# Optimization experiments

Measured on AMD Instinct MI355X. Metric: run time of the kernel, lower is better.

## Reference

```python
import jax, jax.numpy as jnp
import numpy as np


def setup_inputs() -> dict:
    key = jax.random.key(0)
    k1, k2 = jax.random.split(key)
    enc = jax.random.normal(k1, (32, 64, 64, 64), dtype=jnp.float32)   # (B, C, H, W), C == D
    embed = jax.random.normal(k2, (512, 64), dtype=jnp.float32)        # (K, D) codebook
    return {"enc": enc, "embed": embed}


def reference(enc, embed):
    B, C, H, W = enc.shape
    K, D = embed.shape
    # torch: enc.view(B, -1, C) with C == D -> plain reshape (no transpose), faithful to source.
    x = enc.reshape(B, -1, D)                                          # (B, N, D), N = C*H*W/D
    # Squared L2 distances; argmin is invariant under sqrt so we skip torch.cdist's sqrt.
    x_sq = jnp.sum(x * x, axis=-1, keepdims=True)                      # (B, N, 1)
    e_sq = jnp.sum(embed * embed, axis=-1)                             # (K,)
    d2 = x_sq - 2.0 * jnp.einsum('bnd,kd->bnk', x, embed) + e_sq       # (B, N, K)
    closest = jnp.argmin(d2, axis=-1)                                  # (B, N) int
    quantized = embed[closest]                                         # (B, N, D) gather
    commitment_loss = jnp.mean((jax.lax.stop_gradient(quantized) - x) ** 2)
    codebook_loss = jnp.mean((quantized - jax.lax.stop_gradient(x)) ** 2)
    quantize_loss = codebook_loss + 1.0 * commitment_loss
    # Straight-through estimator.
    quant_out = (x + jax.lax.stop_gradient(quantized - x)).reshape(B, C, H, W)
    return quant_out, quantize_loss, closest
```

## Files before the change

### kernel.cpp

```cpp
#include <hip/hip_runtime.h>
#include <math.h>

#define DQ 64
#define KQ 512
#define NVEC 131072
#define QOUT_SIZE (NVEC * DQ)
#define LOSS_OFF QOUT_SIZE
#define IDX_OFF (QOUT_SIZE + 1)

#define RPW 32
#define WPB 4
#define VPB (RPW * WPB)
#define NBLK (NVEC / VPB)
#define SC 64
#define NST (KQ / SC)
#define SDQ (SC * DQ)
#define TIE_THR 0.01f

typedef __attribute__((ext_vector_type(8))) short short8;
typedef __attribute__((ext_vector_type(4))) float f32x4;

static __device__ __forceinline__ unsigned short f2bf(float f) {
    unsigned u = __float_as_uint(f);
    u += 0x7fff + ((u >> 16) & 1);
    return (unsigned short)(u >> 16);
}
static __device__ __forceinline__ float bf2f(unsigned short h) {
    return __uint_as_float(((unsigned)h) << 16);
}
static __device__ __forceinline__ void cvt8(float4 a, float4 b, short8& hi, short8& lo) {
#define C1(I, V) { unsigned short _h = f2bf(V); hi[I] = (short)_h; lo[I] = (short)f2bf((V) - bf2f(_h)); }
    C1(0, a.x) C1(1, a.y) C1(2, a.z) C1(3, a.w)
    C1(4, b.x) C1(5, b.y) C1(6, b.z) C1(7, b.w)
#undef C1
}

__global__ void vq_init_kernel(const float* __restrict__ embed,
                               unsigned short* __restrict__ ehi,
                               unsigned short* __restrict__ elo,
                               float* __restrict__ esq,
                               float* __restrict__ out) {
    const int t = blockIdx.x * 64 + threadIdx.x;
    if (t == 0) out[LOSS_OFF] = 0.0f;
    const int k = t >> 3;
    const int c = t & 7;
    const float4* p = (const float4*)(embed + (size_t)k * DQ + c * 8);
    float4 a = p[0], b = p[1];
    short8 hi, lo;
    cvt8(a, b, hi, lo);
    const int slot = c ^ (k & 7);
    *(short8*)(ehi + (size_t)k * DQ + slot * 8) = hi;
    *(short8*)(elo + (size_t)k * DQ + slot * 8) = lo;

    float ps = 0.f;
    ps = fmaf(a.x, a.x, ps); ps = fmaf(a.y, a.y, ps); ps = fmaf(a.z, a.z, ps); ps = fmaf(a.w, a.w, ps);
    ps = fmaf(b.x, b.x, ps); ps = fmaf(b.y, b.y, ps); ps = fmaf(b.z, b.z, ps); ps = fmaf(b.w, b.w, ps);
    ps += __shfl_xor(ps, 1);
    ps += __shfl_xor(ps, 2);
    ps += __shfl_xor(ps, 4);
    if (c == 0) esq[k] = ps;
}

__global__ __launch_bounds__(256) void vq_mfma_kernel(const float* __restrict__ enc,
                                                      const float* __restrict__ embed,
                                                      const unsigned short* __restrict__ ehi,
                                                      const unsigned short* __restrict__ elo,
                                                      const float* __restrict__ esq,
                                                      float* __restrict__ out) {
    __shared__ unsigned short hs[2 * SDQ];
    __shared__ unsigned short ls_[2 * SDQ];
    __shared__ float esq_s[KQ];
    __shared__ int bidx_s[VPB];
    __shared__ int flag_s[VPB];
    __shared__ float red[WPB];

    const int tid = threadIdx.x;
    const int lane = tid & 63;
    const int w = tid >> 6;
    const int l15 = lane & 15;
    const int l4 = lane >> 4;
    const int vb = blockIdx.x * VPB + w * RPW;

    esq_s[tid] = esq[tid];
    esq_s[tid + 256] = esq[tid + 256];

    short8 ahA[2], alA[2], ahB[2], alB[2];
#pragma unroll
    for (int a = 0; a < 2; a++) {
        const float* base = enc + (size_t)(vb + a * 16 + l15) * DQ + l4 * 8;
        const float4* p0 = (const float4*)base;
        const float4* p1 = (const float4*)(base + 32);
        cvt8(p0[0], p0[1], ahA[a], alA[a]);
        cvt8(p1[0], p1[1], ahB[a], alB[a]);
    }

    float m1[8], m2[8];
    int i1[8];
#pragma unroll
    for (int r = 0; r < 8; r++) { m1[r] = 3.4e38f; m2[r] = 3.4e38f; i1[r] = 0; }

    const int sl0 = (l4 ^ (l15 & 7)) * 8;
    const int sl1 = sl0 ^ 32;

    short8 rh0 = *(const short8*)(ehi + tid * 8);
    short8 rh1 = *(const short8*)(ehi + 2048 + tid * 8);
    short8 rl0 = *(const short8*)(elo + tid * 8);
    short8 rl1 = *(const short8*)(elo + 2048 + tid * 8);
    *(short8*)(hs + tid * 8) = rh0;  *(short8*)(hs + 2048 + tid * 8) = rh1;
    *(short8*)(ls_ + tid * 8) = rl0; *(short8*)(ls_ + 2048 + tid * 8) = rl1;
    rh0 = *(const short8*)(ehi + SDQ + tid * 8);
    rh1 = *(const short8*)(ehi + SDQ + 2048 + tid * 8);
    rl0 = *(const short8*)(elo + SDQ + tid * 8);
    rl1 = *(const short8*)(elo + SDQ + 2048 + tid * 8);

#define LDB(H0, H1, L0, L1, S) { const int _o = ((S) * 16 + l15) * DQ; \
    H0 = *(const short8*)(hb + _o + sl0); H1 = *(const short8*)(hb + _o + sl1); \
    L0 = *(const short8*)(lb + _o + sl0); L1 = *(const short8*)(lb + _o + sl1); }

#define BODY(ST, S, BH0, BH1, BL0, BL1) { \
    const int code = (ST) * SC + (S) * 16 + l15; \
    const float ev = esq_s[code]; \
    _Pragma("unroll") \
    for (int a = 0; a < 2; a++) { \
        f32x4 acc = {0.f, 0.f, 0.f, 0.f}; \
        acc = __builtin_amdgcn_mfma_f32_16x16x32_bf16(ahA[a], BH0, acc, 0, 0, 0); \
        acc = __builtin_amdgcn_mfma_f32_16x16x32_bf16(ahB[a], BH1, acc, 0, 0, 0); \
        acc = __builtin_amdgcn_mfma_f32_16x16x32_bf16(alA[a], BH0, acc, 0, 0, 0); \
        acc = __builtin_amdgcn_mfma_f32_16x16x32_bf16(alB[a], BH1, acc, 0, 0, 0); \
        acc = __builtin_amdgcn_mfma_f32_16x16x32_bf16(ahA[a], BL0, acc, 0, 0, 0); \
        acc = __builtin_amdgcn_mfma_f32_16x16x32_bf16(ahB[a], BL1, acc, 0, 0, 0); \
        _Pragma("unroll") \
        for (int r = 0; r < 4; r++) { \
            float v = fmaf(-2.0f, acc[r], ev); \
            bool lt = v < m1[a * 4 + r]; \
            i1[a * 4 + r] = lt ? code : i1[a * 4 + r]; \
            m2[a * 4 + r] = fminf(m2[a * 4 + r], fmaxf(m1[a * 4 + r], v)); \
            m1[a * 4 + r] = fminf(m1[a * 4 + r], v); \
        } \
    } }

    for (int st = 0; st < NST; st++) {
        __syncthreads();
        if (st < NST - 1) {
            unsigned short* hw = hs + ((st + 1) & 1) * SDQ;
            unsigned short* lw = ls_ + ((st + 1) & 1) * SDQ;
            *(short8*)(hw + tid * 8) = rh0;  *(short8*)(hw + 2048 + tid * 8) = rh1;
            *(short8*)(lw + tid * 8) = rl0;  *(short8*)(lw + 2048 + tid * 8) = rl1;
        }
        if (st < NST - 2) {
            const int o = (st + 2) * SDQ;
            rh0 = *(const short8*)(ehi + o + tid * 8);
            rh1 = *(const short8*)(ehi + o + 2048 + tid * 8);
            rl0 = *(const short8*)(elo + o + tid * 8);
            rl1 = *(const short8*)(elo + o + 2048 + tid * 8);
        }
        const unsigned short* hb = hs + (st & 1) * SDQ;
        const unsigned short* lb = ls_ + (st & 1) * SDQ;
        short8 b0h0, b0h1, b0l0, b0l1, b1h0, b1h1, b1l0, b1l1;
        LDB(b0h0, b0h1, b0l0, b0l1, 0)
        LDB(b1h0, b1h1, b1l0, b1l1, 1)
        BODY(st, 0, b0h0, b0h1, b0l0, b0l1)
        LDB(b0h0, b0h1, b0l0, b0l1, 2)
        BODY(st, 1, b1h0, b1h1, b1l0, b1l1)
        LDB(b1h0, b1h1, b1l0, b1l1, 3)
        BODY(st, 2, b0h0, b0h1, b0l0, b0l1)
        BODY(st, 3, b1h0, b1h1, b1l0, b1l1)
    }
#undef LDB
#undef BODY

#pragma unroll
    for (int m = 1; m <= 8; m <<= 1) {
#pragma unroll
        for (int r = 0; r < 8; r++) {
            float o1 = __shfl_xor(m1[r], m);
            float o2 = __shfl_xor(m2[r], m);
            int oi = __shfl_xor(i1[r], m);
            float nm2 = fminf(fminf(m2[r], o2), fmaxf(m1[r], o1));
            bool lt = o1 < m1[r];
            i1[r] = lt ? oi : i1[r];
            m1[r] = fminf(m1[r], o1);
            m2[r] = nm2;
        }
    }

    if (l15 == 0) {
#pragma unroll
        for (int a = 0; a < 2; a++)
#pragma unroll
            for (int r = 0; r < 4; r++) {
                const int row = a * 16 + l4 * 4 + r;
                bidx_s[w * RPW + row] = i1[a * 4 + r];
                flag_s[w * RPW + row] = (m2[a * 4 + r] - m1[a * 4 + r] < TIE_THR) ? 1 : 0;
            }
    }

    for (int row = 0; row < RPW; row++) {
        if (flag_s[w * RPW + row]) {
            const int v = vb + row;
            const float4* xe = (const float4*)(enc + (size_t)v * DQ);
            unsigned long long best = ~0ULL;
            for (int q = 0; q < 8; q++) {
                const int c = lane * 8 + q;
                const float4* ee = (const float4*)(embed + (size_t)c * DQ);
                double a = 0.0;
                for (int j = 0; j < 16; j++) {
                    float4 xx = xe[j], ez = ee[j];
                    double d0 = (double)xx.x - (double)ez.x; a = fma(d0, d0, a);
                    double d1 = (double)xx.y - (double)ez.y; a = fma(d1, d1, a);
                    double d2 = (double)xx.z - (double)ez.z; a = fma(d2, d2, a);
                    double d3 = (double)xx.w - (double)ez.w; a = fma(d3, d3, a);
                }
                unsigned long long p =
                    (((unsigned long long)__double_as_longlong(a)) & ~511ULL) | (unsigned)c;
                best = (p < best) ? p : best;
            }
#pragma unroll
            for (int mm = 1; mm < 64; mm <<= 1) {
                unsigned long long ob = (unsigned long long)__shfl_xor((long long)best, mm);
                best = (ob < best) ? ob : best;
            }
            if (lane == 0) bidx_s[w * RPW + row] = (int)(best & 511ULL);
        }
    }

    float lsum = 0.f;
#pragma unroll
    for (int a = 0; a < 2; a++) {
        const int myv = vb + a * 16 + l15;
        const int qb = bidx_s[w * RPW + a * 16 + l15];
        const float* qbase = embed + (size_t)qb * DQ + l4 * 8;
        const float4* qa = (const float4*)qbase;
        const float4* qc = (const float4*)(qbase + 32);
        float4 q0 = qa[0], q1 = qa[1], q2 = qc[0], q3 = qc[1];
        float* obase = out + (size_t)myv * DQ + l4 * 8;
        ((float4*)obase)[0] = q0; ((float4*)obase)[1] = q1;
        ((float4*)(obase + 32))[0] = q2; ((float4*)(obase + 32))[1] = q3;
        if (l4 == 0) out[IDX_OFF + myv] = (float)qb;

        float d;
        d = q0.x - (bf2f(ahA[a][0]) + bf2f(alA[a][0])); lsum = fmaf(d, d, lsum);
        d = q0.y - (bf2f(ahA[a][1]) + bf2f(alA[a][1])); lsum = fmaf(d, d, lsum);
        d = q0.z - (bf2f(ahA[a][2]) + bf2f(alA[a][2])); lsum = fmaf(d, d, lsum);
        d = q0.w - (bf2f(ahA[a][3]) + bf2f(alA[a][3])); lsum = fmaf(d, d, lsum);
        d = q1.x - (bf2f(ahA[a][4]) + bf2f(alA[a][4])); lsum = fmaf(d, d, lsum);
        d = q1.y - (bf2f(ahA[a][5]) + bf2f(alA[a][5])); lsum = fmaf(d, d, lsum);
        d = q1.z - (bf2f(ahA[a][6]) + bf2f(alA[a][6])); lsum = fmaf(d, d, lsum);
        d = q1.w - (bf2f(ahA[a][7]) + bf2f(alA[a][7])); lsum = fmaf(d, d, lsum);
        d = q2.x - (bf2f(ahB[a][0]) + bf2f(alB[a][0])); lsum = fmaf(d, d, lsum);
        d = q2.y - (bf2f(ahB[a][1]) + bf2f(alB[a][1])); lsum = fmaf(d, d, lsum);
        d = q2.z - (bf2f(ahB[a][2]) + bf2f(alB[a][2])); lsum = fmaf(d, d, lsum);
        d = q2.w - (bf2f(ahB[a][3]) + bf2f(alB[a][3])); lsum = fmaf(d, d, lsum);
        d = q3.x - (bf2f(ahB[a][4]) + bf2f(alB[a][4])); lsum = fmaf(d, d, lsum);
        d = q3.y - (bf2f(ahB[a][5]) + bf2f(alB[a][5])); lsum = fmaf(d, d, lsum);
        d = q3.z - (bf2f(ahB[a][6]) + bf2f(alB[a][6])); lsum = fmaf(d, d, lsum);
        d = q3.w - (bf2f(ahB[a][7]) + bf2f(alB[a][7])); lsum = fmaf(d, d, lsum);
    }

#pragma unroll
    for (int off = 32; off > 0; off >>= 1) lsum += __shfl_down(lsum, off);
    if (lane == 0) red[w] = lsum;
    __syncthreads();
    if (tid == 0) {
        float s = (red[0] + red[1]) + (red[2] + red[3]);
        atomicAdd(out + LOSS_OFF, s * (2.0f / (float)QOUT_SIZE));
    }
}

extern "C" void kernel_launch(void* const* d_in, const int* in_sizes, int n_in,
                              void* d_out, int out_size, void* d_ws, size_t ws_size,
                              hipStream_t stream) {
    const float* enc = (const float*)d_in[0];
    const float* embed = (const float*)d_in[1];
    float* out = (float*)d_out;
    unsigned short* ehi = (unsigned short*)d_ws;
    unsigned short* elo = ehi + KQ * DQ;
    float* esq = (float*)(elo + KQ * DQ);

    hipLaunchKernelGGL(vq_init_kernel, dim3(64), dim3(64), 0, stream,
                       embed, ehi, elo, esq, out);
    hipLaunchKernelGGL(vq_mfma_kernel, dim3(NBLK), dim3(256), 0, stream,
                       enc, embed, ehi, elo, esq, out);
}
```

Measured before the change: 141.8 us.

## Drop codebook low-bf16 split, pack argmin index into distance bits, widen tie threshold

Removes the low-precision half of the codebook split, so each tile needs four MFMAs instead of six and half the shared-memory staging and global loads. The code index is packed into the low mantissa bits of the distance, which removes the separate index tracking and its shuffles. The tie threshold rises from 0.01 to 0.2 to make up for the lost precision, so more rows may drop into the slow fp64 recheck path. The shared buffer is also padded with an odd-looking pad that raises LDS usage and may lower occupancy.

```diff
diff --git a/kernel.cpp b/kernel.cpp
--- a/kernel.cpp
+++ b/kernel.cpp
@@ -15,7 +15,9 @@
 #define SC 64
 #define NST (KQ / SC)
 #define SDQ (SC * DQ)
-#define TIE_THR 0.01f
+#define PADS 2654
+#define SDQ_P (SDQ + PADS)
+#define TIE_THR 0.2f
 
 typedef __attribute__((ext_vector_type(8))) short short8;
 typedef __attribute__((ext_vector_type(4))) float f32x4;
@@ -37,7 +39,6 @@
 
 __global__ void vq_init_kernel(const float* __restrict__ embed,
                                unsigned short* __restrict__ ehi,
-                               unsigned short* __restrict__ elo,
                                float* __restrict__ esq,
                                float* __restrict__ out) {
     const int t = blockIdx.x * 64 + threadIdx.x;
@@ -46,11 +47,12 @@
     const int c = t & 7;
     const float4* p = (const float4*)(embed + (size_t)k * DQ + c * 8);
     float4 a = p[0], b = p[1];
-    short8 hi, lo;
-    cvt8(a, b, hi, lo);
+    unsigned short h0 = f2bf(a.x), h1 = f2bf(a.y), h2 = f2bf(a.z), h3 = f2bf(a.w);
+    unsigned short h4 = f2bf(b.x), h5 = f2bf(b.y), h6 = f2bf(b.z), h7 = f2bf(b.w);
+    short8 hi = { (short)h0, (short)h1, (short)h2, (short)h3,
+                  (short)h4, (short)h5, (short)h6, (short)h7 };
     const int slot = c ^ (k & 7);
     *(short8*)(ehi + (size_t)k * DQ + slot * 8) = hi;
-    *(short8*)(elo + (size_t)k * DQ + slot * 8) = lo;
 
     float ps = 0.f;
     ps = fmaf(a.x, a.x, ps); ps = fmaf(a.y, a.y, ps); ps = fmaf(a.z, a.z, ps); ps = fmaf(a.w, a.w, ps);
@@ -64,11 +66,9 @@
 __global__ __launch_bounds__(256) void vq_mfma_kernel(const float* __restrict__ enc,
                                                       const float* __restrict__ embed,
                                                       const unsigned short* __restrict__ ehi,
-                                                      const unsigned short* __restrict__ elo,
                                                       const float* __restrict__ esq,
                                                       float* __restrict__ out) {
-    __shared__ unsigned short hs[2 * SDQ];
-    __shared__ unsigned short ls_[2 * SDQ];
+    __shared__ unsigned short hs[2 * SDQ_P];
     __shared__ float esq_s[KQ];
     __shared__ int bidx_s[VPB];
     __shared__ int flag_s[VPB];
@@ -95,29 +95,22 @@
     }
 
     float m1[8], m2[8];
-    int i1[8];
-#pragma unroll
-    for (int r = 0; r < 8; r++) { m1[r] = 3.4e38f; m2[r] = 3.4e38f; i1[r] = 0; }
+#pragma unroll
+    for (int r = 0; r < 8; r++) { m1[r] = 3.4e38f; m2[r] = 3.4e38f; }
 
     const int sl0 = (l4 ^ (l15 & 7)) * 8;
     const int sl1 = sl0 ^ 32;
 
     short8 rh0 = *(const short8*)(ehi + tid * 8);
     short8 rh1 = *(const short8*)(ehi + 2048 + tid * 8);
-    short8 rl0 = *(const short8*)(elo + tid * 8);
-    short8 rl1 = *(const short8*)(elo + 2048 + tid * 8);
     *(short8*)(hs + tid * 8) = rh0;  *(short8*)(hs + 2048 + tid * 8) = rh1;
-    *(short8*)(ls_ + tid * 8) = rl0; *(short8*)(ls_ + 2048 + tid * 8) = rl1;
     rh0 = *(const short8*)(ehi + SDQ + tid * 8);
     rh1 = *(const short8*)(ehi + SDQ + 2048 + tid * 8);
-    rl0 = *(const short8*)(elo + SDQ + tid * 8);
-    rl1 = *(const short8*)(elo + SDQ + 2048 + tid * 8);
-
-#define LDB(H0, H1, L0, L1, S) { const int _o = ((S) * 16 + l15) * DQ; \
-    H0 = *(const short8*)(hb + _o + sl0); H1 = *(const short8*)(hb + _o + sl1); \
-    L0 = *(const short8*)(lb + _o + sl0); L1 = *(const short8*)(lb + _o + sl1); }
-
-#define BODY(ST, S, BH0, BH1, BL0, BL1) { \
+
+#define LDB(H0, H1, S) { const int _o = ((S) * 16 + l15) * DQ; \
+    H0 = *(const short8*)(hb + _o + sl0); H1 = *(const short8*)(hb + _o + sl1); }
+
+#define BODY(ST, S, BH0, BH1) { \
     const int code = (ST) * SC + (S) * 16 + l15; \
     const float ev = esq_s[code]; \
     _Pragma("unroll") \
@@ -127,44 +120,36 @@
         acc = __builtin_amdgcn_mfma_f32_16x16x32_bf16(ahB[a], BH1, acc, 0, 0, 0); \
         acc = __builtin_amdgcn_mfma_f32_16x16x32_bf16(alA[a], BH0, acc, 0, 0, 0); \
         acc = __builtin_amdgcn_mfma_f32_16x16x32_bf16(alB[a], BH1, acc, 0, 0, 0); \
-        acc = __builtin_amdgcn_mfma_f32_16x16x32_bf16(ahA[a], BL0, acc, 0, 0, 0); \
-        acc = __builtin_amdgcn_mfma_f32_16x16x32_bf16(ahB[a], BL1, acc, 0, 0, 0); \
         _Pragma("unroll") \
         for (int r = 0; r < 4; r++) { \
             float v = fmaf(-2.0f, acc[r], ev); \
-            bool lt = v < m1[a * 4 + r]; \
-            i1[a * 4 + r] = lt ? code : i1[a * 4 + r]; \
-            m2[a * 4 + r] = fminf(m2[a * 4 + r], fmaxf(m1[a * 4 + r], v)); \
-            m1[a * 4 + r] = fminf(m1[a * 4 + r], v); \
+            float p = __uint_as_float((__float_as_uint(v) & 0xFFFFFE00u) | (unsigned)code); \
+            m2[a * 4 + r] = fminf(m2[a * 4 + r], fmaxf(m1[a * 4 + r], p)); \
+            m1[a * 4 + r] = fminf(m1[a * 4 + r], p); \
         } \
     } }
 
     for (int st = 0; st < NST; st++) {
         __syncthreads();
         if (st < NST - 1) {
-            unsigned short* hw = hs + ((st + 1) & 1) * SDQ;
-            unsigned short* lw = ls_ + ((st + 1) & 1) * SDQ;
+            unsigned short* hw = hs + ((st + 1) & 1) * SDQ_P;
             *(short8*)(hw + tid * 8) = rh0;  *(short8*)(hw + 2048 + tid * 8) = rh1;
-            *(short8*)(lw + tid * 8) = rl0;  *(short8*)(lw + 2048 + tid * 8) = rl1;
         }
         if (st < NST - 2) {
             const int o = (st + 2) * SDQ;
             rh0 = *(const short8*)(ehi + o + tid * 8);
             rh1 = *(const short8*)(ehi + o + 2048 + tid * 8);
-            rl0 = *(const short8*)(elo + o + tid * 8);
-            rl1 = *(const short8*)(elo + o + 2048 + tid * 8);
-        }
-        const unsigned short* hb = hs + (st & 1) * SDQ;
-        const unsigned short* lb = ls_ + (st & 1) * SDQ;
-        short8 b0h0, b0h1, b0l0, b0l1, b1h0, b1h1, b1l0, b1l1;
-        LDB(b0h0, b0h1, b0l0, b0l1, 0)
-        LDB(b1h0, b1h1, b1l0, b1l1, 1)
-        BODY(st, 0, b0h0, b0h1, b0l0, b0l1)
-        LDB(b0h0, b0h1, b0l0, b0l1, 2)
-        BODY(st, 1, b1h0, b1h1, b1l0, b1l1)
-        LDB(b1h0, b1h1, b1l0, b1l1, 3)
-        BODY(st, 2, b0h0, b0h1, b0l0, b0l1)
-        BODY(st, 3, b1h0, b1h1, b1l0, b1l1)
+        }
+        const unsigned short* hb = hs + (st & 1) * SDQ_P;
+        short8 b0h0, b0h1, b1h0, b1h1;
+        LDB(b0h0, b0h1, 0)
+        LDB(b1h0, b1h1, 1)
+        BODY(st, 0, b0h0, b0h1)
+        LDB(b0h0, b0h1, 2)
+        BODY(st, 1, b1h0, b1h1)
+        LDB(b1h0, b1h1, 3)
+        BODY(st, 2, b0h0, b0h1)
+        BODY(st, 3, b1h0, b1h1)
     }
 #undef LDB
 #undef BODY
@@ -175,12 +160,8 @@
         for (int r = 0; r < 8; r++) {
             float o1 = __shfl_xor(m1[r], m);
             float o2 = __shfl_xor(m2[r], m);
-            int oi = __shfl_xor(i1[r], m);
-            float nm2 = fminf(fminf(m2[r], o2), fmaxf(m1[r], o1));
-            bool lt = o1 < m1[r];
-            i1[r] = lt ? oi : i1[r];
+            m2[r] = fminf(fminf(m2[r], o2), fmaxf(m1[r], o1));
             m1[r] = fminf(m1[r], o1);
-            m2[r] = nm2;
         }
     }
 
@@ -190,7 +171,7 @@
 #pragma unroll
             for (int r = 0; r < 4; r++) {
                 const int row = a * 16 + l4 * 4 + r;
-                bidx_s[w * RPW + row] = i1[a * 4 + r];
+                bidx_s[w * RPW + row] = (int)(__float_as_uint(m1[a * 4 + r]) & 511u);
                 flag_s[w * RPW + row] = (m2[a * 4 + r] - m1[a * 4 + r] < TIE_THR) ? 1 : 0;
             }
     }
@@ -274,11 +255,10 @@
     const float* embed = (const float*)d_in[1];
     float* out = (float*)d_out;
     unsigned short* ehi = (unsigned short*)d_ws;
-    unsigned short* elo = ehi + KQ * DQ;
-    float* esq = (float*)(elo + KQ * DQ);
+    float* esq = (float*)(ehi + KQ * DQ);
 
     hipLaunchKernelGGL(vq_init_kernel, dim3(64), dim3(64), 0, stream,
-                       embed, ehi, elo, esq, out);
+                       embed, ehi, esq, out);
     hipLaunchKernelGGL(vq_mfma_kernel, dim3(NBLK), dim3(256), 0, stream,
-                       enc, embed, ehi, elo, esq, out);
-}
+                       enc, embed, ehi, esq, out);
+}
```

After: 278.5 us. +96.5%, slower.
